# Optimization experiments

Hardware: AMD Instinct MI355X
Metric: run time of the kernel (lower is better)

The kernel has to match this reference:

```python
import jax, jax.numpy as jnp
import numpy as np

EPS = 1e-9
NEG = -99.0


def setup_inputs() -> dict:
    key = jax.random.key(0)
    k1, k2 = jax.random.split(key)
    N, D, LEN_PRD = 8192, 512, 4096
    embeddings = jax.random.normal(k1, (N, D), dtype=jnp.float32)
    W = jax.random.randint(k2, (N, N), 0, 2, dtype=jnp.int32)
    return {"embeddings": embeddings, "W": W, "len_prd": LEN_PRD, "head": 1}


def reference(embeddings, W, len_prd, head):
    # mask = -99 * (1 - W_block)
    Wb = (W[:len_prd, len_prd:] if head == 1 else W).astype(jnp.float32)
    mask = NEG * (1.0 - Wb)

    # row-normalize embeddings with eps clamp on norms
    norms = jnp.linalg.norm(embeddings, axis=1, keepdims=True)
    norms = jnp.where(norms <= EPS, EPS, norms)
    ne = embeddings / norms

    # cosine similarity; when head==1 only the [:len_prd, len_prd:] block is
    # kept, so compute just that block (same math as full matmul + slice)
    if head == 1:
        sim = ne[:len_prd] @ ne[len_prd:].T  # [len_prd, N-len_prd]
    else:
        sim = ne @ ne.T

    masked = sim + mask

    # output_matrix = clamp(relu(masked), max=1)
    output_matrix = jnp.minimum(jnp.maximum(masked, 0.0), 1.0)

    # half_normalized = 1 / (1 - masked); row-sum normalize with eps clamp
    half = 1.0 / (1.0 - masked)
    row_sum = jnp.sum(half, axis=1, keepdims=True)
    row_sum = jnp.where(row_sum <= EPS, EPS, row_sum)
    normed = half / row_sum

    # supple flag: 1 if no positive entry in the masked row, else 0;
    # zero out flagged rows and append the flag as an extra column
    supple = jnp.where(jnp.any(masked > 0.0, axis=1), 0.0, 1.0)  # [x_len]
    processed = jnp.where(supple[:, None] == 1.0, 0.0, normed)
    extended = jnp.concatenate([processed, supple[:, None]], axis=1)

    return (output_matrix, extended)
```

## Files before the change

### kernel.cpp

```cpp
#include <hip/hip_runtime.h>
#include <hip/hip_bf16.h>
#include <stdint.h>

#define NROW 8192
#define DIM  512
#define LP   4096
#define NB   4096
#define EXTW 4097
#define NEGC (-99.0f)
#define EPSF 1e-9f

typedef __attribute__((ext_vector_type(8))) __bf16 bf16x8;
typedef __attribute__((ext_vector_type(4))) float f32x4;

__global__ __launch_bounds__(256) void k_norm(const float* __restrict__ emb,
                                              __hip_bfloat16* __restrict__ ne) {
    const int row = blockIdx.x;
    const int t = threadIdx.x;
    const float* rp = emb + (size_t)row * DIM;
    float2 v = *(const float2*)(rp + t * 2);
    float s = v.x * v.x + v.y * v.y;
    #pragma unroll
    for (int off = 32; off; off >>= 1) s += __shfl_down(s, off);
    __shared__ float wsum[4];
    const int wid = t >> 6, lane = t & 63;
    if (lane == 0) wsum[wid] = s;
    __syncthreads();
    float tot = wsum[0] + wsum[1] + wsum[2] + wsum[3];
    float nrm = sqrtf(tot);
    nrm = (nrm <= EPSF) ? EPSF : nrm;
    const float inv = 1.0f / nrm;
    __hip_bfloat162 pk;
    pk.x = __float2bfloat16(v.x * inv);
    pk.y = __float2bfloat16(v.y * inv);
    *(__hip_bfloat162*)(ne + (size_t)row * DIM + t * 2) = pk;
}

#define BM 128
#define BN 128
#define BK 64
#define SIMLD 132

#define GLOAD_LDS(gp, lp) __builtin_amdgcn_global_load_lds(                     \
    (const __attribute__((address_space(1))) uint32_t*)(gp),                    \
    (__attribute__((address_space(3))) uint32_t*)(lp), 16, 0, 0)

__global__ __launch_bounds__(256) void k_gemm(const __hip_bfloat16* __restrict__ ne,
                                              const int* __restrict__ W,
                                              float* __restrict__ out0,
                                              __hip_bfloat16* __restrict__ half16,
                                              float* __restrict__ psum,
                                              int* __restrict__ pany) {
    __shared__ __align__(16) char smem[32768];
    __bf16* As = (__bf16*)smem;
    __bf16* Bs = (__bf16*)(smem + 16384);
    float*  Sim = (float*)smem;

    const int bid = blockIdx.x;
    const int wg = (bid & 7) * 128 + (bid >> 3);
    const int tileR = wg >> 5, tileC = wg & 31;

    const int tid = threadIdx.x;
    const int lane = tid & 63, wid = tid >> 6;
    const int wr = wid >> 1, wc = wid & 1;
    const int r16 = lane & 15, kg = lane >> 4;

    const __bf16* A = (const __bf16*)ne + (size_t)(tileR * BM) * DIM;
    const __bf16* B = (const __bf16*)ne + (size_t)(LP + tileC * BN) * DIM;

    const int srow = lane >> 3;
    const int scol = (((lane & 7) ^ srow) << 3);

    f32x4 acc[4][4] = {};

    for (int kt = 0; kt < 8; ++kt) {
        const int k0 = kt * BK;
        #pragma unroll
        for (int i = 0; i < 4; ++i) {
            const int seg = wid * 4 + i;
            const int r = seg * 8 + srow;
            GLOAD_LDS(A + (size_t)r * DIM + k0 + scol, As + seg * 512);
            GLOAD_LDS(B + (size_t)r * DIM + k0 + scol, Bs + seg * 512);
        }
        __syncthreads();
        #pragma unroll
        for (int kk = 0; kk < 2; ++kk) {
            bf16x8 af[4], bfr[4];
            #pragma unroll
            for (int m = 0; m < 4; ++m) {
                const int ra = wr * 64 + m * 16 + r16;
                af[m] = *(const bf16x8*)(As + ra * 64 + ((kk * 32 + kg * 8) ^ ((ra & 7) << 3)));
            }
            #pragma unroll
            for (int n = 0; n < 4; ++n) {
                const int rb = wc * 64 + n * 16 + r16;
                bfr[n] = *(const bf16x8*)(Bs + rb * 64 + ((kk * 32 + kg * 8) ^ ((rb & 7) << 3)));
            }
            #pragma unroll
            for (int m = 0; m < 4; ++m)
                #pragma unroll
                for (int n = 0; n < 4; ++n)
                    acc[m][n] = __builtin_amdgcn_mfma_f32_16x16x32_bf16(af[m], bfr[n], acc[m][n], 0, 0, 0);
        }
        __syncthreads();
    }

    const int gr_base = tileR * BM;
    const int gc_base = tileC * BN;
    const int lr = (tid >> 5);
    const int cc = (tid & 31) * 4;

    #pragma unroll
    for (int m = 0; m < 4; ++m) {
        __syncthreads();
        #pragma unroll
        for (int n = 0; n < 4; ++n)
            #pragma unroll
            for (int j = 0; j < 4; ++j)
                Sim[(wr * 16 + kg * 4 + j) * SIMLD + wc * 64 + n * 16 + r16] = acc[m][n][j];
        __syncthreads();
        #pragma unroll
        for (int p = 0; p < 4; ++p) {
            const int r = p * 8 + lr;
            const int gr = gr_base + ((r >> 4) << 6) + m * 16 + (r & 15);
            const int gc = gc_base + cc;
            const float4 s4 = *(const float4*)(Sim + r * SIMLD + cc);
            const int4 w4 = *(const int4*)(W + (size_t)gr * NROW + LP + gc);
            const float m0 = w4.x ? s4.x : (s4.x + NEGC);
            const float m1 = w4.y ? s4.y : (s4.y + NEGC);
            const float m2 = w4.z ? s4.z : (s4.z + NEGC);
            const float m3 = w4.w ? s4.w : (s4.w + NEGC);
            float4 o;
            o.x = fminf(fmaxf(m0, 0.0f), 1.0f);
            o.y = fminf(fmaxf(m1, 0.0f), 1.0f);
            o.z = fminf(fmaxf(m2, 0.0f), 1.0f);
            o.w = fminf(fmaxf(m3, 0.0f), 1.0f);
            *(float4*)(out0 + (size_t)gr * NB + gc) = o;
            const float h0 = 1.0f / (1.0f - m0);
            const float h1 = 1.0f / (1.0f - m1);
            const float h2 = 1.0f / (1.0f - m2);
            const float h3 = 1.0f / (1.0f - m3);
            __hip_bfloat16 hp[4] = {__float2bfloat16(h0), __float2bfloat16(h1),
                                    __float2bfloat16(h2), __float2bfloat16(h3)};
            *(ushort4*)(half16 + (size_t)gr * NB + gc) = *(const ushort4*)hp;
            float ps = (h0 + h1) + (h2 + h3);
            int pa = (m0 > 0.0f) | (m1 > 0.0f) | (m2 > 0.0f) | (m3 > 0.0f);
            #pragma unroll
            for (int off = 1; off < 32; off <<= 1) {
                ps += __shfl_xor(ps, off);
                pa |= __shfl_xor(pa, off);
            }
            if ((tid & 31) == 0) {
                psum[(size_t)gr * 32 + tileC] = ps;
                pany[(size_t)gr * 32 + tileC] = pa;
            }
        }
    }
}

__global__ __launch_bounds__(256) void k_final(const __hip_bfloat16* __restrict__ half16,
                                               const float* __restrict__ psum,
                                               const int* __restrict__ pany,
                                               float* __restrict__ ext) {
    const int row = blockIdx.x;
    const int t = threadIdx.x;
    __shared__ float sInv;
    __shared__ int sAny;
    if (t < 64) {
        float s = (t < 32) ? psum[(size_t)row * 32 + t] : 0.0f;
        int a = (t < 32) ? pany[(size_t)row * 32 + t] : 0;
        #pragma unroll
        for (int off = 16; off; off >>= 1) {
            s += __shfl_xor(s, off);
            a |= __shfl_xor(a, off);
        }
        if (t == 0) {
            float tot = (s <= EPSF) ? EPSF : s;
            sInv = a ? (1.0f / tot) : 0.0f;
            sAny = a;
        }
    }
    __syncthreads();
    const float inv = sInv;
    const uint16_t* hp = (const uint16_t*)(half16 + (size_t)row * NB);
    float* rp = ext + (size_t)row * EXTW;
    #pragma unroll
    for (int i = 0; i < 16; ++i) {
        const int c = t + i * 256;
        const uint32_t u = (uint32_t)hp[c] << 16;
        rp[c] = __uint_as_float(u) * inv;
    }
    if (t == 0) rp[NB] = sAny ? 0.0f : 1.0f;
}

extern "C" void kernel_launch(void* const* d_in, const int* in_sizes, int n_in,
                              void* d_out, int out_size, void* d_ws, size_t ws_size,
                              hipStream_t stream) {
    const float* emb = (const float*)d_in[0];
    const int* W = (const int*)d_in[1];

    float* out0 = (float*)d_out;
    float* ext = (float*)d_out + (size_t)LP * NB;
    __hip_bfloat16* ne = (__hip_bfloat16*)d_ws;
    __hip_bfloat16* half16 = (__hip_bfloat16*)((char*)d_ws + ((size_t)16 << 20));
    float* psum = (float*)((char*)d_ws + ((size_t)48 << 20));
    int*   pany = (int*)((char*)d_ws + ((size_t)49 << 20));

    k_norm<<<dim3(NROW), dim3(256), 0, stream>>>(emb, ne);
    k_gemm<<<dim3((LP / BM) * (NB / BN)), dim3(256), 0, stream>>>(ne, W, out0, half16, psum, pany);
    k_final<<<dim3(LP), dim3(256), 0, stream>>>(half16, psum, pany, ext);
}
```

Baseline: 78.79 us.

## Fuse row-normalization pass into GEMM via per-row-tile atomic barrier

Removes the separate k_final kernel. Each GEMM block now increments a per-row-tile counter and spins until all 32 column tiles of that row band have written their partial sums. It then reduces psum/pany for its 128 rows and writes its own normalized tile of the extended output. This saves a kernel launch and the re-read pass, at the cost of spin-waiting. It relies on all blocks of a row band being co-resident (a deadlock risk if they are not), and its ext writes are 2-element scalar stores that are poorly coalesced.

```diff
diff --git a/kernel.cpp b/kernel.cpp
--- a/kernel.cpp
+++ b/kernel.cpp
@@ -48,13 +48,17 @@
 __global__ __launch_bounds__(256) void k_gemm(const __hip_bfloat16* __restrict__ ne,
                                               const int* __restrict__ W,
                                               float* __restrict__ out0,
+                                              float* __restrict__ ext,
                                               __hip_bfloat16* __restrict__ half16,
                                               float* __restrict__ psum,
-                                              int* __restrict__ pany) {
-    __shared__ __align__(16) char smem[32768];
+                                              int* __restrict__ pany,
+                                              int* __restrict__ cnt) {
+    __shared__ __align__(16) char smem[33536];
     __bf16* As = (__bf16*)smem;
     __bf16* Bs = (__bf16*)(smem + 16384);
     float*  Sim = (float*)smem;
+    float*  RowS = (float*)(smem + 32768);
+    int*    RowA = (int*)(smem + 33280);
 
     const int bid = blockIdx.x;
     const int wg = (bid & 7) * 128 + (bid >> 3);
@@ -156,41 +160,66 @@
             }
         }
     }
-}
-
-__global__ __launch_bounds__(256) void k_final(const __hip_bfloat16* __restrict__ half16,
-                                               const float* __restrict__ psum,
-                                               const int* __restrict__ pany,
-                                               float* __restrict__ ext) {
-    const int row = blockIdx.x;
-    const int t = threadIdx.x;
-    __shared__ float sInv;
-    __shared__ int sAny;
-    if (t < 64) {
-        float s = (t < 32) ? psum[(size_t)row * 32 + t] : 0.0f;
-        int a = (t < 32) ? pany[(size_t)row * 32 + t] : 0;
-        #pragma unroll
-        for (int off = 16; off; off >>= 1) {
-            s += __shfl_xor(s, off);
-            a |= __shfl_xor(a, off);
-        }
-        if (t == 0) {
-            float tot = (s <= EPSF) ? EPSF : s;
-            sInv = a ? (1.0f / tot) : 0.0f;
-            sAny = a;
-        }
-    }
-    __syncthreads();
-    const float inv = sInv;
-    const uint16_t* hp = (const uint16_t*)(half16 + (size_t)row * NB);
-    float* rp = ext + (size_t)row * EXTW;
-    #pragma unroll
-    for (int i = 0; i < 16; ++i) {
-        const int c = t + i * 256;
-        const uint32_t u = (uint32_t)hp[c] << 16;
-        rp[c] = __uint_as_float(u) * inv;
-    }
-    if (t == 0) rp[NB] = sAny ? 0.0f : 1.0f;
+
+    __threadfence();
+    if (tid == 0) {
+        atomicAdd(&cnt[tileR], 1);
+        while (__hip_atomic_load(&cnt[tileR], __ATOMIC_ACQUIRE,
+                                 __HIP_MEMORY_SCOPE_AGENT) < 32) {
+            __builtin_amdgcn_s_sleep(16);
+        }
+    }
+    __syncthreads();
+
+    if (tid < 128) {
+        const int gr = gr_base + tid;
+        const float4* ps4 = (const float4*)(psum + (size_t)gr * 32);
+        const int4*   pa4 = (const int4*)(pany + (size_t)gr * 32);
+        float s = 0.0f; int a = 0;
+        #pragma unroll
+        for (int j = 0; j < 8; ++j) {
+            const float4 v = ps4[j];
+            s += (v.x + v.y) + (v.z + v.w);
+            const int4 b = pa4[j];
+            a |= b.x | b.y | b.z | b.w;
+        }
+        s = (s <= EPSF) ? EPSF : s;
+        RowS[tid] = a ? (1.0f / s) : 0.0f;
+        if (tid < 64) RowA[tid] = 0;
+    }
+    __syncthreads();
+    if (tid < 128) {
+        const int gr = gr_base + tid;
+        const float4* ps4 = (const float4*)(psum + (size_t)gr * 32);
+        (void)ps4;
+    }
+    __syncthreads();
+
+    const int prow = tid >> 6;
+    const int pc2 = (tid & 63) * 2;
+    #pragma unroll 8
+    for (int i = 0; i < 32; ++i) {
+        const int o = i * 4 + prow;
+        const float inv = RowS[o];
+        const int gr = gr_base + o;
+        const uint16_t* hp = (const uint16_t*)(half16 + (size_t)gr * NB + gc_base + pc2);
+        float* ep = ext + (size_t)gr * EXTW + gc_base + pc2;
+        const uint32_t u0 = (uint32_t)hp[0] << 16;
+        const uint32_t u1 = (uint32_t)hp[1] << 16;
+        ep[0] = __uint_as_float(u0) * inv;
+        ep[1] = __uint_as_float(u1) * inv;
+    }
+    if (tileC == 31 && tid < 128) {
+        const int gr = gr_base + tid;
+        const int4* pa4 = (const int4*)(pany + (size_t)gr * 32);
+        int a = 0;
+        #pragma unroll
+        for (int j = 0; j < 8; ++j) {
+            const int4 b = pa4[j];
+            a |= b.x | b.y | b.z | b.w;
+        }
+        ext[(size_t)gr * EXTW + NB] = a ? 0.0f : 1.0f;
+    }
 }
 
 extern "C" void kernel_launch(void* const* d_in, const int* in_sizes, int n_in,
@@ -205,8 +234,10 @@
     __hip_bfloat16* half16 = (__hip_bfloat16*)((char*)d_ws + ((size_t)16 << 20));
     float* psum = (float*)((char*)d_ws + ((size_t)48 << 20));
     int*   pany = (int*)((char*)d_ws + ((size_t)49 << 20));
-
+    int*   cnt  = (int*)((char*)d_ws + ((size_t)50 << 20));
+
+    hipMemsetAsync(cnt, 0, 32 * sizeof(int), stream);
     k_norm<<<dim3(NROW), dim3(256), 0, stream>>>(emb, ne);
-    k_gemm<<<dim3((LP / BM) * (NB / BN)), dim3(256), 0, stream>>>(ne, W, out0, half16, psum, pany);
-    k_final<<<dim3(LP), dim3(256), 0, stream>>>(half16, psum, pany, ext);
+    k_gemm<<<dim3((LP / BM) * (NB / BN)), dim3(256), 0, stream>>>(
+        ne, W, out0, ext, half16, psum, pany, cnt);
 }
```

Measured after the change: 253.9 us. 3.22x slower.
